# Kernel tuning notes

Measured on AMD Instinct MI355X. Metric: run time of the kernel, lower is better.

Reference implementation:

```python
import jax, jax.numpy as jnp
import numpy as np
import math

HIDDEN = 2048
NUM_HEADS = 16
HEAD_DIM = HIDDEN // NUM_HEADS  # 128
B, T = 2, 2048
MAX_POS = 4096
ROPE_BASE = 10000.0


def _rope_cache(dim, max_pos, base):
    inv_freq = 1.0 / (base ** (jnp.arange(0, dim, 2, dtype=jnp.float32) / dim))
    t = jnp.arange(max_pos, dtype=jnp.float32)
    freqs = jnp.einsum('i,j->ij', t, inv_freq)        # [max_pos, dim/2]
    emb = jnp.concatenate([freqs, freqs], axis=-1)     # [max_pos, dim]
    return jnp.cos(emb), jnp.sin(emb)


def setup_inputs() -> dict:
    key = jax.random.key(0)
    ks = jax.random.split(key, 5)
    hidden_states = jax.random.normal(ks[0], (B, T, HIDDEN), dtype=jnp.float32)
    # additive causal mask, large negative (not -inf) for numerical safety
    causal = jnp.triu(jnp.full((T, T), -1e9, dtype=jnp.float32), k=1)
    attention_mask = causal[None, None, :, :]          # [1,1,T,T]
    position_ids = jnp.arange(T, dtype=jnp.int64)
    s = 1.0 / math.sqrt(HIDDEN)
    Wq = jax.random.normal(ks[1], (HIDDEN, HIDDEN), dtype=jnp.float32) * s
    Wk = jax.random.normal(ks[2], (HIDDEN, HIDDEN), dtype=jnp.float32) * s
    Wv = jax.random.normal(ks[3], (HIDDEN, HIDDEN), dtype=jnp.float32) * s
    Wo = jax.random.normal(ks[4], (HIDDEN, HIDDEN), dtype=jnp.float32) * s
    cos_cached, sin_cached = _rope_cache(HEAD_DIM, MAX_POS, ROPE_BASE)
    return {
        'hidden_states': hidden_states,
        'attention_mask': attention_mask,
        'position_ids': position_ids,
        'Wq': Wq, 'Wk': Wk, 'Wv': Wv, 'Wo': Wo,
        'cos_cached': cos_cached, 'sin_cached': sin_cached,
    }


def _apply_rope(x, cos, sin):
    # x: [B, T, nh, hd]; cos/sin: [T, 1, hd] (broadcast over heads)
    x1 = x[..., 0::2]
    x2 = x[..., 1::2]
    x_rot = jnp.stack([-x2, x1], axis=-1).reshape(x.shape)  # interleaved rotate
    return x * cos + x_rot * sin


def reference(hidden_states, attention_mask, position_ids, Wq, Wk, Wv, Wo,
              cos_cached, sin_cached):
    Bs, Ts, H = hidden_states.shape
    nh, hd = NUM_HEADS, HEAD_DIM
    q = (hidden_states @ Wq.T).reshape(Bs, Ts, nh, hd)
    k = (hidden_states @ Wk.T).reshape(Bs, Ts, nh, hd)
    v = (hidden_states @ Wv.T).reshape(Bs, Ts, nh, hd)
    cos = cos_cached[position_ids][:, None, :]  # [T,1,hd]
    sin = sin_cached[position_ids][:, None, :]
    q = _apply_rope(q, cos, sin)
    k = _apply_rope(k, cos, sin)
    # [B, nh, T, hd]
    q = q.transpose(0, 2, 1, 3)
    k = k.transpose(0, 2, 1, 3)
    v = v.transpose(0, 2, 1, 3)
    scores = jnp.einsum('bhqd,bhkd->bhqk', q, k) / math.sqrt(hd)
    scores = scores + attention_mask
    attn = jax.nn.softmax(scores, axis=-1)
    out = jnp.einsum('bhqk,bhkd->bhqd', attn, v)
    out = out.transpose(0, 2, 1, 3).reshape(Bs, Ts, H)
    return out @ Wo.T
```

## Files before the change

### kernel.cpp

```cpp
#include <hip/hip_runtime.h>
#include <cstdint>


typedef __bf16 v8bf __attribute__((ext_vector_type(8)));
typedef float  v4f  __attribute__((ext_vector_type(4)));
typedef float  f32x16 __attribute__((ext_vector_type(16)));

__device__ __forceinline__ uint16_t f2bf(float f) {
  union { float f; uint32_t u; } v; v.f = f;
  uint32_t u = v.u;
  return (uint16_t)((u + 0x7FFFu + ((u >> 16) & 1u)) >> 16);
}

__device__ __forceinline__ uint32_t cvtpk(float lo, float hi) {
  uint32_t w;
  asm("v_cvt_pk_bf16_f32 %0, %1, %2" : "=v"(w) : "v"(lo), "v"(hi));
  return w;
}

__device__ __forceinline__ void gload16(const void* g, void* l) {
  __builtin_amdgcn_global_load_lds(
      (const __attribute__((address_space(1))) void*)g,
      (__attribute__((address_space(3))) void*)l, 16, 0, 0);
}

__global__ void cvt_all_kernel(const float* __restrict__ s0, uint16_t* d0,
                               const float* __restrict__ s1, uint16_t* d1,
                               const float* __restrict__ s2, uint16_t* d2,
                               const float* __restrict__ s3, uint16_t* d3,
                               const float* __restrict__ s4, uint16_t* d4) {
  const float* src; uint16_t* dst; int n4;
  switch (blockIdx.y) {
    case 0: src = s0; dst = d0; n4 = 2097152; break;
    case 1: src = s1; dst = d1; n4 = 1048576; break;
    case 2: src = s2; dst = d2; n4 = 1048576; break;
    case 3: src = s3; dst = d3; n4 = 1048576; break;
    default: src = s4; dst = d4; n4 = 1048576; break;
  }
  int i = blockIdx.x * blockDim.x + threadIdx.x;
  int stride = gridDim.x * blockDim.x;
  for (; i < n4; i += stride) {
    float4 v = reinterpret_cast<const float4*>(src)[i];
    ushort4 o;
    o.x = f2bf(v.x); o.y = f2bf(v.y); o.z = f2bf(v.z); o.w = f2bf(v.w);
    reinterpret_cast<ushort4*>(dst)[i] = o;
  }
}

__device__ __forceinline__ void gemm128_mainloop(
    const uint16_t* __restrict__ A, const uint16_t* __restrict__ Bt,
    int m0, int n0, uint16_t* As, uint16_t* Bs, v4f acc[4][4]) {
  const int tid  = threadIdx.x;
  const int lane = tid & 63;
  const int w    = tid >> 6;
  const int wr   = w >> 1, wc = w & 1;
  const int lrow = lane & 15;
  const int lhi  = lane >> 4;

  auto stage = [&](int buf, int k0) {
    uint16_t* Ad = As + buf * 8192;
    uint16_t* Bd = Bs + buf * 8192;
#pragma unroll
    for (int i = 0; i < 4; ++i) {
      int c = i * 256 + tid;
      int row = c >> 3, seg = c & 7;
      int sseg = seg ^ (row & 7);
      gload16(A + (size_t)(m0 + row) * 2048 + k0 + sseg * 8, Ad + c * 8);
    }
#pragma unroll
    for (int i = 0; i < 4; ++i) {
      int c = i * 256 + tid;
      int row = c >> 3, seg = c & 7;
      int sseg = seg ^ (row & 7);
      gload16(Bt + (size_t)(n0 + row) * 2048 + k0 + sseg * 8, Bd + c * 8);
    }
  };

  stage(0, 0);
  for (int t = 0; t < 32; ++t) {
    __syncthreads();
    if (t + 1 < 32) stage((t + 1) & 1, (t + 1) * 64);
    const uint16_t* Ac = As + (t & 1) * 8192;
    const uint16_t* Bc = Bs + (t & 1) * 8192;
#pragma unroll
    for (int ks = 0; ks < 2; ++ks) {
      v8bf af[4], bfv[4];
#pragma unroll
      for (int mf = 0; mf < 4; ++mf) {
        const int ar = wr * 64 + mf * 16 + lrow;
        const int seg = (ks * 4 + lhi) ^ (ar & 7);
        af[mf] = *reinterpret_cast<const v8bf*>(Ac + ar * 64 + seg * 8);
      }
#pragma unroll
      for (int nf = 0; nf < 4; ++nf) {
        const int br = wc * 64 + nf * 16 + lrow;
        const int seg = (ks * 4 + lhi) ^ (br & 7);
        bfv[nf] = *reinterpret_cast<const v8bf*>(Bc + br * 64 + seg * 8);
      }
#pragma unroll
      for (int mf = 0; mf < 4; ++mf)
#pragma unroll
        for (int nf = 0; nf < 4; ++nf)
          acc[mf][nf] = __builtin_amdgcn_mfma_f32_16x16x32_bf16(
              af[mf], bfv[nf], acc[mf][nf], 0, 0, 0);
    }
  }
}

__global__ __launch_bounds__(256, 2) void qkv_gemm_kernel(
    const uint16_t* __restrict__ Xbf,
    const uint16_t* __restrict__ Wqb, const uint16_t* __restrict__ Wkb,
    const uint16_t* __restrict__ Wvb,
    const float* __restrict__ cosc, const float* __restrict__ sinc,
    uint16_t* __restrict__ Qh, uint16_t* __restrict__ Kh,
    uint16_t* __restrict__ Vt) {
  __shared__ uint16_t As[2 * 128 * 64];
  __shared__ uint16_t Bs[2 * 128 * 64];
  const int id  = (blockIdx.z * 32 + blockIdx.y) * 16 + blockIdx.x;
  const int swz = (id & 7) * 192 + (id >> 3);
  const int which = swz >> 9;
  const int m0 = ((swz >> 4) & 31) * 128, n0 = (swz & 15) * 128;
  const uint16_t* Wb = (which == 0) ? Wqb : (which == 1) ? Wkb : Wvb;

  v4f acc[4][4];
#pragma unroll
  for (int i = 0; i < 4; ++i)
#pragma unroll
    for (int j = 0; j < 4; ++j) acc[i][j] = (v4f)0.0f;

  gemm128_mainloop(Xbf, Wb, m0, n0, As, Bs, acc);

  const int lane = threadIdx.x & 63;
  const int w = threadIdx.x >> 6, wr = w >> 1, wc = w & 1;
  const int lrow = lane & 15, lhi = lane >> 4;
  const int b = m0 >> 11;

  if (which < 2) {
    uint16_t* dst = (which == 0) ? Qh : Kh;
#pragma unroll
    for (int mf = 0; mf < 4; ++mf) {
#pragma unroll
      for (int nf = 0; nf < 4; ++nf) {
        const int n = n0 + wc * 64 + nf * 16 + lrow;
        const int head = n >> 7, d = n & 127;
#pragma unroll
        for (int r = 0; r < 4; ++r) {
          const int m = m0 + wr * 64 + mf * 16 + lhi * 4 + r;
          const int t = m & 2047;
          float v = acc[mf][nf][r];
          float p = __shfl_xor(v, 1);
          float rot = (n & 1) ? p : -p;
          float cf = cosc[t * 128 + d], sf = sinc[t * 128 + d];
          dst[((size_t)(b * 16 + head) * 2048 + t) * 128 + d] =
              f2bf(v * cf + rot * sf);
        }
      }
    }
  } else {
#pragma unroll
    for (int mf = 0; mf < 4; ++mf) {
#pragma unroll
      for (int nf = 0; nf < 4; ++nf) {
        const int n = n0 + wc * 64 + nf * 16 + lrow;
        const int head = n >> 7, d = n & 127;
        const int m = m0 + wr * 64 + mf * 16 + lhi * 4;
        const int t = m & 2047;
        ushort4 o;
        o.x = f2bf(acc[mf][nf][0]); o.y = f2bf(acc[mf][nf][1]);
        o.z = f2bf(acc[mf][nf][2]); o.w = f2bf(acc[mf][nf][3]);
        *reinterpret_cast<ushort4*>(
            &Vt[((size_t)(b * 16 + head) * 128 + d) * 2048 + t]) = o;
      }
    }
  }
}

__global__ __launch_bounds__(256, 2) void attn_kernel(
    const uint16_t* __restrict__ Qh, const uint16_t* __restrict__ Kh,
    const uint16_t* __restrict__ Vt, uint16_t* __restrict__ Ob) {
  __shared__ uint16_t Ks[2 * 64 * 128];
  __shared__ uint16_t Vs[2 * 128 * 64];

  const int id = blockIdx.x;
  const int qt = (id < 256) ? (15 - (id >> 5)) : ((id - 256) >> 5);
  const int bh = id & 31;
  const int tid = threadIdx.x, lane = tid & 63, w = tid >> 6;
  const int l31 = lane & 31, hi = lane >> 5;
  const size_t base = (size_t)bh * 2048 * 128;
  const int q0 = qt * 128 + w * 32;
  const int qr = q0 + l31;

  v8bf qf[8];
#pragma unroll
  for (int ks = 0; ks < 8; ++ks)
    qf[ks] = *reinterpret_cast<const v8bf*>(
        Qh + base + (size_t)qr * 128 + ks * 16 + hi * 8);

  f32x16 acc[4];
#pragma unroll
  for (int d = 0; d < 4; ++d) acc[d] = (f32x16)0.0f;
  float m = -1e30f, l = 0.0f;

  auto stage = [&](int buf, int kt) {
    uint16_t* Kd = Ks + buf * 8192;
    uint16_t* Vd = Vs + buf * 8192;
#pragma unroll
    for (int i = 0; i < 4; ++i) {
      int c = i * 256 + tid;
      int row = c >> 4, seg = c & 15;
      int sseg = seg ^ (row & 7);
      gload16(Kh + base + (size_t)(kt * 64 + row) * 128 + sseg * 8,
              Kd + c * 8);
    }
#pragma unroll
    for (int i = 0; i < 4; ++i) {
      int c = i * 256 + tid;
      int row = c >> 3, seg = c & 7;
      int sseg = seg ^ (row & 7);
      gload16(Vt + base + (size_t)row * 2048 + kt * 64 + sseg * 8,
              Vd + c * 8);
    }
  };

  const float sc = 0.08838834764831845f;
  const int nkt = 2 * (qt + 1);
  stage(0, 0);
  for (int kt = 0; kt < nkt; ++kt) {
    const int cur = kt & 1;
    __syncthreads();
    if (kt + 1 < nkt) stage(cur ^ 1, kt + 1);
    const uint16_t* Kc = Ks + cur * 8192;
    const uint16_t* Vc = Vs + cur * 8192;

    if (kt * 64 <= q0 + 31) {
      f32x16 s[2];
      s[0] = (f32x16)0.0f; s[1] = (f32x16)0.0f;
#pragma unroll
      for (int kb = 0; kb < 2; ++kb) {
        const int row = kb * 32 + l31;
        const int swz = row & 7;
#pragma unroll
        for (int ks = 0; ks < 8; ++ks) {
          const int seg = (ks * 2 + hi) ^ swz;
          v8bf kf = *reinterpret_cast<const v8bf*>(Kc + row * 128 + seg * 8);
          s[kb] = __builtin_amdgcn_mfma_f32_32x32x16_bf16(kf, qf[ks], s[kb],
                                                          0, 0, 0);
        }
      }
      if (kt * 64 + 63 > q0) {
#pragma unroll
        for (int kb = 0; kb < 2; ++kb)
#pragma unroll
          for (int q = 0; q < 4; ++q)
#pragma unroll
            for (int r = 0; r < 4; ++r) {
              const int kc = kt * 64 + kb * 32 + q * 8 + hi * 4 + r;
              float v = s[kb][q * 4 + r] * sc;
              s[kb][q * 4 + r] = (kc > qr) ? -1e30f : v;
            }
      } else {
#pragma unroll
        for (int kb = 0; kb < 2; ++kb)
#pragma unroll
          for (int g = 0; g < 16; ++g) s[kb][g] *= sc;
      }
      float t8[8];
#pragma unroll
      for (int g = 0; g < 8; ++g)
        t8[g] = fmaxf(fmaxf(s[0][g], s[0][g + 8]),
                      fmaxf(s[1][g], s[1][g + 8]));
      float mx = fmaxf(fmaxf(fmaxf(t8[0], t8[1]), fmaxf(t8[2], t8[3])),
                       fmaxf(fmaxf(t8[4], t8[5]), fmaxf(t8[6], t8[7])));
      mx = fmaxf(mx, __shfl_xor(mx, 32));
      if (!__all(mx - m <= 8.0f)) {
        const float mnew = fmaxf(m, mx);
        const float so = __expf(m - mnew);
        m = mnew;
        l *= so;
#pragma unroll
        for (int d = 0; d < 4; ++d)
#pragma unroll
          for (int g = 0; g < 16; ++g) acc[d][g] *= so;
      }
      float rs = 0.0f;
#pragma unroll
      for (int kb = 0; kb < 2; ++kb)
#pragma unroll
        for (int g = 0; g < 16; ++g) {
          const float pv = __expf(s[kb][g] - m);
          s[kb][g] = pv;
          rs += pv;
        }
      rs += __shfl_xor(rs, 32);
      l += rs;
      union BW { uint32_t w[4]; v8bf v; };
      BW pb[4];
#pragma unroll
      for (int kb = 0; kb < 2; ++kb)
#pragma unroll
        for (int sl = 0; sl < 2; ++sl) {
          uint32_t a0 = cvtpk(s[kb][8 * sl + 0], s[kb][8 * sl + 1]);
          uint32_t a1 = cvtpk(s[kb][8 * sl + 2], s[kb][8 * sl + 3]);
          uint32_t b0 = cvtpk(s[kb][8 * sl + 4], s[kb][8 * sl + 5]);
          uint32_t b1 = cvtpk(s[kb][8 * sl + 6], s[kb][8 * sl + 7]);
          asm("v_permlane32_swap_b32 %0, %1" : "+v"(a0), "+v"(b0));
          asm("v_permlane32_swap_b32 %0, %1" : "+v"(a1), "+v"(b1));
          BW& f = pb[kb * 2 + sl];
          f.w[0] = a0; f.w[1] = a1; f.w[2] = b0; f.w[3] = b1;
        }
#pragma unroll
      for (int d = 0; d < 4; ++d) {
        const int row = d * 32 + l31;
        const int swz = row & 7;
#pragma unroll
        for (int sl4 = 0; sl4 < 4; ++sl4) {
          const int seg = (sl4 * 2 + hi) ^ swz;
          v8bf va = *reinterpret_cast<const v8bf*>(Vc + row * 64 + seg * 8);
          acc[d] = __builtin_amdgcn_mfma_f32_32x32x16_bf16(va, pb[sl4].v,
                                                           acc[d], 0, 0, 0);
        }
      }
    }
  }

  const int b = bh >> 4, head = bh & 15;
  const float inv = 1.0f / l;
#pragma unroll
  for (int d = 0; d < 4; ++d)
#pragma unroll
    for (int q = 0; q < 4; ++q)
#pragma unroll
      for (int rp = 0; rp < 2; ++rp) {
        const int dd = d * 32 + q * 8 + hi * 4 + rp * 2;
        const uint32_t lo16 = f2bf(acc[d][q * 4 + rp * 2] * inv);
        const uint32_t hi16 = f2bf(acc[d][q * 4 + rp * 2 + 1] * inv);
        *reinterpret_cast<uint32_t*>(
            &Ob[((size_t)(b * 2048 + qr)) * 2048 + head * 128 + dd]) =
            lo16 | (hi16 << 16);
      }
}

__global__ __launch_bounds__(256, 2) void out_gemm_kernel(
    const uint16_t* __restrict__ Abf, const uint16_t* __restrict__ Wob,
    float* __restrict__ out) {
  __shared__ uint16_t As[2 * 128 * 64];
  __shared__ uint16_t Bs[2 * 128 * 64];
  const int id  = blockIdx.y * 16 + blockIdx.x;
  const int swz = (id & 7) * 64 + (id >> 3);
  const int m0 = (swz >> 4) * 128, n0 = (swz & 15) * 128;
  v4f acc[4][4];
#pragma unroll
  for (int i = 0; i < 4; ++i)
#pragma unroll
    for (int j = 0; j < 4; ++j) acc[i][j] = (v4f)0.0f;

  gemm128_mainloop(Abf, Wob, m0, n0, As, Bs, acc);

  const int lane = threadIdx.x & 63;
  const int w = threadIdx.x >> 6, wr = w >> 1, wc = w & 1;
  const int lrow = lane & 15, lhi = lane >> 4;
#pragma unroll
  for (int mf = 0; mf < 4; ++mf)
#pragma unroll
    for (int nf = 0; nf < 4; ++nf) {
      const int n = n0 + wc * 64 + nf * 16 + lrow;
#pragma unroll
      for (int r = 0; r < 4; ++r) {
        const int m = m0 + wr * 64 + mf * 16 + lhi * 4 + r;
        out[(size_t)m * 2048 + n] = acc[mf][nf][r];
      }
    }
}

extern "C" void kernel_launch(void* const* d_in, const int* in_sizes, int n_in,
                              void* d_out, int out_size, void* d_ws,
                              size_t ws_size, hipStream_t stream) {
  const float* hidden = (const float*)d_in[0];
  const float* Wq = (const float*)d_in[3];
  const float* Wk = (const float*)d_in[4];
  const float* Wv = (const float*)d_in[5];
  const float* Wo = (const float*)d_in[6];
  const float* cosc = (const float*)d_in[7];
  const float* sinc = (const float*)d_in[8];
  float* out = (float*)d_out;

  uint16_t* Wqb = (uint16_t*)d_ws;
  uint16_t* Wkb = Wqb + 4194304;
  uint16_t* Wvb = Wkb + 4194304;
  uint16_t* Wob = Wvb + 4194304;
  uint16_t* Xbf = Wob + 4194304;
  uint16_t* Qh  = Xbf + 8388608;
  uint16_t* Kh  = Qh + 8388608;
  uint16_t* Vt  = Kh + 8388608;
  uint16_t* Ob  = Xbf;

  cvt_all_kernel<<<dim3(512, 5), 256, 0, stream>>>(
      hidden, Xbf, Wq, Wqb, Wk, Wkb, Wv, Wvb, Wo, Wob);

  qkv_gemm_kernel<<<dim3(16, 32, 3), 256, 0, stream>>>(
      Xbf, Wqb, Wkb, Wvb, cosc, sinc, Qh, Kh, Vt);

  attn_kernel<<<dim3(512), 256, 0, stream>>>(Qh, Kh, Vt, Ob);

  out_gemm_kernel<<<dim3(16, 32), 256, 0, stream>>>(Ob, Wob, out);
}
```

Before: 408.9 us.

## Enlarge GEMM tiles with triple-buffered pipeline; shrink attention KV tiles and stage output via LDS

The GEMMs switch to 256x128 tiles with 512 threads and a three-stage LDS ring. Loads are split across the two k-substeps with explicit vmcnt waits, barriers and setprio around the MFMA block, to overlap global loads with compute and raise reuse. Attention moves to 32-key tiles with a three-buffer ring and explicit waitcnt. Its output goes through a swizzled LDS transpose so each row is written to global memory in coalesced form. The risks are higher LDS use limiting occupancy (the GEMMs need 144KB of LDS at 2 blocks per CU), and more barrier overhead per attention tile.

New measurement: 381.2 us. 1.07x faster.

```diff
diff --git a/kernel.cpp b/kernel.cpp
--- a/kernel.cpp
+++ b/kernel.cpp
@@ -47,79 +47,104 @@
   }
 }
 
-__device__ __forceinline__ void gemm128_mainloop(
+__device__ __forceinline__ void gemm256_mainloop(
     const uint16_t* __restrict__ A, const uint16_t* __restrict__ Bt,
     int m0, int n0, uint16_t* As, uint16_t* Bs, v4f acc[4][4]) {
   const int tid  = threadIdx.x;
-  const int lane = tid & 63;
-  const int w    = tid >> 6;
-  const int wr   = w >> 1, wc = w & 1;
-  const int lrow = lane & 15;
-  const int lhi  = lane >> 4;
-
-  auto stage = [&](int buf, int k0) {
-    uint16_t* Ad = As + buf * 8192;
-    uint16_t* Bd = Bs + buf * 8192;
-#pragma unroll
-    for (int i = 0; i < 4; ++i) {
-      int c = i * 256 + tid;
-      int row = c >> 3, seg = c & 7;
-      int sseg = seg ^ (row & 7);
-      gload16(A + (size_t)(m0 + row) * 2048 + k0 + sseg * 8, Ad + c * 8);
-    }
-#pragma unroll
-    for (int i = 0; i < 4; ++i) {
-      int c = i * 256 + tid;
-      int row = c >> 3, seg = c & 7;
-      int sseg = seg ^ (row & 7);
-      gload16(Bt + (size_t)(n0 + row) * 2048 + k0 + sseg * 8, Bd + c * 8);
-    }
+  const int lane = tid & 63, w = tid >> 6;
+  const int wm = w >> 1, wn = w & 1;
+  const int lrow = lane & 15, lhi = lane >> 4;
+
+  auto stageA = [&](int buf, int k0, int i) {
+    int c = i * 512 + tid;
+    int row = c >> 3, seg = c & 7;
+    int sseg = seg ^ (row & 7);
+    gload16(A + (size_t)(m0 + row) * 2048 + k0 + sseg * 8,
+            As + buf * 16384 + c * 8);
   };
-
-  stage(0, 0);
+  auto stageB = [&](int buf, int k0, int i) {
+    int c = i * 512 + tid;
+    int row = c >> 3, seg = c & 7;
+    int sseg = seg ^ (row & 7);
+    gload16(Bt + (size_t)(n0 + row) * 2048 + k0 + sseg * 8,
+            Bs + buf * 8192 + c * 8);
+  };
+
+#pragma unroll
+  for (int i = 0; i < 4; ++i) stageA(0, 0, i);
+#pragma unroll
+  for (int i = 0; i < 2; ++i) stageB(0, 0, i);
+#pragma unroll
+  for (int i = 0; i < 4; ++i) stageA(1, 64, i);
+#pragma unroll
+  for (int i = 0; i < 2; ++i) stageB(1, 64, i);
+  asm volatile("s_waitcnt vmcnt(6)" ::: "memory");
+  __builtin_amdgcn_s_barrier();
+  __builtin_amdgcn_sched_barrier(0);
+
   for (int t = 0; t < 32; ++t) {
-    __syncthreads();
-    if (t + 1 < 32) stage((t + 1) & 1, (t + 1) * 64);
-    const uint16_t* Ac = As + (t & 1) * 8192;
-    const uint16_t* Bc = Bs + (t & 1) * 8192;
+    const int cb = t % 3;
+    const int sb = (t + 2) % 3;
+    const int sk = (t + 2) * 64;
+    const uint16_t* Ac = As + cb * 16384;
+    const uint16_t* Bc = Bs + cb * 8192;
+    const bool do_stage = (t + 2) < 32;
 #pragma unroll
     for (int ks = 0; ks < 2; ++ks) {
       v8bf af[4], bfv[4];
 #pragma unroll
       for (int mf = 0; mf < 4; ++mf) {
-        const int ar = wr * 64 + mf * 16 + lrow;
+        const int ar = wm * 64 + mf * 16 + lrow;
         const int seg = (ks * 4 + lhi) ^ (ar & 7);
         af[mf] = *reinterpret_cast<const v8bf*>(Ac + ar * 64 + seg * 8);
       }
 #pragma unroll
       for (int nf = 0; nf < 4; ++nf) {
-        const int br = wc * 64 + nf * 16 + lrow;
+        const int br = wn * 64 + nf * 16 + lrow;
         const int seg = (ks * 4 + lhi) ^ (br & 7);
         bfv[nf] = *reinterpret_cast<const v8bf*>(Bc + br * 64 + seg * 8);
       }
+      if (do_stage) {
+        if (ks == 0) { stageA(sb, sk, 0); stageA(sb, sk, 1); stageB(sb, sk, 0); }
+        else         { stageA(sb, sk, 2); stageA(sb, sk, 3); stageB(sb, sk, 1); }
+      }
+      if (ks == 1) {
+        if (t < 30) asm volatile("s_waitcnt vmcnt(6)" ::: "memory");
+        else        asm volatile("s_waitcnt vmcnt(0)" ::: "memory");
+      } else {
+        asm volatile("" ::: "memory");
+      }
+      __builtin_amdgcn_s_barrier();
+      __builtin_amdgcn_sched_barrier(0);
+      __builtin_amdgcn_s_setprio(1);
 #pragma unroll
       for (int mf = 0; mf < 4; ++mf)
 #pragma unroll
         for (int nf = 0; nf < 4; ++nf)
           acc[mf][nf] = __builtin_amdgcn_mfma_f32_16x16x32_bf16(
               af[mf], bfv[nf], acc[mf][nf], 0, 0, 0);
-    }
-  }
-}
-
-__global__ __launch_bounds__(256, 2) void qkv_gemm_kernel(
+      __builtin_amdgcn_s_setprio(0);
+      asm volatile("" ::: "memory");
+      __builtin_amdgcn_s_barrier();
+      __builtin_amdgcn_sched_barrier(0);
+    }
+  }
+}
+
+__global__ __launch_bounds__(512, 2) void qkv_gemm_kernel(
     const uint16_t* __restrict__ Xbf,
     const uint16_t* __restrict__ Wqb, const uint16_t* __restrict__ Wkb,
     const uint16_t* __restrict__ Wvb,
     const float* __restrict__ cosc, const float* __restrict__ sinc,
     uint16_t* __restrict__ Qh, uint16_t* __restrict__ Kh,
     uint16_t* __restrict__ Vt) {
-  __shared__ uint16_t As[2 * 128 * 64];
-  __shared__ uint16_t Bs[2 * 128 * 64];
-  const int id  = (blockIdx.z * 32 + blockIdx.y) * 16 + blockIdx.x;
-  const int swz = (id & 7) * 192 + (id >> 3);
-  const int which = swz >> 9;
-  const int m0 = ((swz >> 4) & 31) * 128, n0 = (swz & 15) * 128;
+  __shared__ uint16_t As[3 * 256 * 64];
+  __shared__ uint16_t Bs[3 * 128 * 64];
+  const int id  = blockIdx.x;
+  const int swz = (id & 7) * 96 + (id >> 3);
+  const int which = swz >> 8;
+  const int rem = swz & 255;
+  const int m0 = (rem >> 4) * 256, n0 = (rem & 15) * 128;
   const uint16_t* Wb = (which == 0) ? Wqb : (which == 1) ? Wkb : Wvb;
 
   v4f acc[4][4];
@@ -128,10 +153,10 @@
 #pragma unroll
     for (int j = 0; j < 4; ++j) acc[i][j] = (v4f)0.0f;
 
-  gemm128_mainloop(Xbf, Wb, m0, n0, As, Bs, acc);
+  gemm256_mainloop(Xbf, Wb, m0, n0, As, Bs, acc);
 
   const int lane = threadIdx.x & 63;
-  const int w = threadIdx.x >> 6, wr = w >> 1, wc = w & 1;
+  const int w = threadIdx.x >> 6, wm = w >> 1, wn = w & 1;
   const int lrow = lane & 15, lhi = lane >> 4;
   const int b = m0 >> 11;
 
@@ -141,11 +166,11 @@
     for (int mf = 0; mf < 4; ++mf) {
 #pragma unroll
       for (int nf = 0; nf < 4; ++nf) {
-        const int n = n0 + wc * 64 + nf * 16 + lrow;
+        const int n = n0 + wn * 64 + nf * 16 + lrow;
         const int head = n >> 7, d = n & 127;
 #pragma unroll
         for (int r = 0; r < 4; ++r) {
-          const int m = m0 + wr * 64 + mf * 16 + lhi * 4 + r;
+          const int m = m0 + wm * 64 + mf * 16 + lhi * 4 + r;
           const int t = m & 2047;
           float v = acc[mf][nf][r];
           float p = __shfl_xor(v, 1);
@@ -161,9 +186,9 @@
     for (int mf = 0; mf < 4; ++mf) {
 #pragma unroll
       for (int nf = 0; nf < 4; ++nf) {
-        const int n = n0 + wc * 64 + nf * 16 + lrow;
+        const int n = n0 + wn * 64 + nf * 16 + lrow;
         const int head = n >> 7, d = n & 127;
-        const int m = m0 + wr * 64 + mf * 16 + lhi * 4;
+        const int m = m0 + wm * 64 + mf * 16 + lhi * 4;
         const int t = m & 2047;
         ushort4 o;
         o.x = f2bf(acc[mf][nf][0]); o.y = f2bf(acc[mf][nf][1]);
@@ -178,8 +203,7 @@
 __global__ __launch_bounds__(256, 2) void attn_kernel(
     const uint16_t* __restrict__ Qh, const uint16_t* __restrict__ Kh,
     const uint16_t* __restrict__ Vt, uint16_t* __restrict__ Ob) {
-  __shared__ uint16_t Ks[2 * 64 * 128];
-  __shared__ uint16_t Vs[2 * 128 * 64];
+  __shared__ uint16_t KV[3][8192];
 
   const int id = blockIdx.x;
   const int qt = (id < 256) ? (15 - (id >> 5)) : ((id - 256) >> 5);
@@ -202,73 +226,67 @@
   float m = -1e30f, l = 0.0f;
 
   auto stage = [&](int buf, int kt) {
-    uint16_t* Kd = Ks + buf * 8192;
-    uint16_t* Vd = Vs + buf * 8192;
-#pragma unroll
-    for (int i = 0; i < 4; ++i) {
+    uint16_t* Kd = KV[buf];
+    uint16_t* Vd = KV[buf] + 4096;
+#pragma unroll
+    for (int i = 0; i < 2; ++i) {
       int c = i * 256 + tid;
       int row = c >> 4, seg = c & 15;
       int sseg = seg ^ (row & 7);
-      gload16(Kh + base + (size_t)(kt * 64 + row) * 128 + sseg * 8,
+      gload16(Kh + base + (size_t)(kt * 32 + row) * 128 + sseg * 8,
               Kd + c * 8);
     }
 #pragma unroll
-    for (int i = 0; i < 4; ++i) {
+    for (int i = 0; i < 2; ++i) {
       int c = i * 256 + tid;
-      int row = c >> 3, seg = c & 7;
-      int sseg = seg ^ (row & 7);
-      gload16(Vt + base + (size_t)row * 2048 + kt * 64 + sseg * 8,
+      int row = c >> 2, seg = c & 3;
+      int sseg = seg ^ (row & 3);
+      gload16(Vt + base + (size_t)row * 2048 + kt * 32 + sseg * 8,
               Vd + c * 8);
     }
   };
 
   const float sc = 0.08838834764831845f;
-  const int nkt = 2 * (qt + 1);
+  const int nkt = 4 * (qt + 1);
   stage(0, 0);
+  stage(1, 1);
   for (int kt = 0; kt < nkt; ++kt) {
-    const int cur = kt & 1;
-    __syncthreads();
-    if (kt + 1 < nkt) stage(cur ^ 1, kt + 1);
-    const uint16_t* Kc = Ks + cur * 8192;
-    const uint16_t* Vc = Vs + cur * 8192;
-
-    if (kt * 64 <= q0 + 31) {
-      f32x16 s[2];
-      s[0] = (f32x16)0.0f; s[1] = (f32x16)0.0f;
-#pragma unroll
-      for (int kb = 0; kb < 2; ++kb) {
-        const int row = kb * 32 + l31;
-        const int swz = row & 7;
+    const int cb = kt % 3;
+    if (kt + 1 < nkt) asm volatile("s_waitcnt vmcnt(4)" ::: "memory");
+    else              asm volatile("s_waitcnt vmcnt(0)" ::: "memory");
+    __builtin_amdgcn_s_barrier();
+    __builtin_amdgcn_sched_barrier(0);
+    if (kt + 2 < nkt) stage((kt + 2) % 3, kt + 2);
+
+    if (kt * 32 <= q0 + 31) {
+      const uint16_t* Kc = KV[cb];
+      const uint16_t* Vc = KV[cb] + 4096;
+      f32x16 s = (f32x16)0.0f;
+      {
+        const int swzk = l31 & 7;
 #pragma unroll
         for (int ks = 0; ks < 8; ++ks) {
-          const int seg = (ks * 2 + hi) ^ swz;
-          v8bf kf = *reinterpret_cast<const v8bf*>(Kc + row * 128 + seg * 8);
-          s[kb] = __builtin_amdgcn_mfma_f32_32x32x16_bf16(kf, qf[ks], s[kb],
-                                                          0, 0, 0);
+          const int seg = (ks * 2 + hi) ^ swzk;
+          v8bf kf = *reinterpret_cast<const v8bf*>(Kc + l31 * 128 + seg * 8);
+          s = __builtin_amdgcn_mfma_f32_32x32x16_bf16(kf, qf[ks], s, 0, 0, 0);
         }
       }
-      if (kt * 64 + 63 > q0) {
-#pragma unroll
-        for (int kb = 0; kb < 2; ++kb)
-#pragma unroll
-          for (int q = 0; q < 4; ++q)
-#pragma unroll
-            for (int r = 0; r < 4; ++r) {
-              const int kc = kt * 64 + kb * 32 + q * 8 + hi * 4 + r;
-              float v = s[kb][q * 4 + r] * sc;
-              s[kb][q * 4 + r] = (kc > qr) ? -1e30f : v;
-            }
+      if (kt * 32 + 31 > q0) {
+#pragma unroll
+        for (int q = 0; q < 4; ++q)
+#pragma unroll
+          for (int r = 0; r < 4; ++r) {
+            const int kc = kt * 32 + q * 8 + hi * 4 + r;
+            float v = s[q * 4 + r] * sc;
+            s[q * 4 + r] = (kc > qr) ? -1e30f : v;
+          }
       } else {
 #pragma unroll
-        for (int kb = 0; kb < 2; ++kb)
-#pragma unroll
-          for (int g = 0; g < 16; ++g) s[kb][g] *= sc;
+        for (int g = 0; g < 16; ++g) s[g] *= sc;
       }
       float t8[8];
 #pragma unroll
-      for (int g = 0; g < 8; ++g)
-        t8[g] = fmaxf(fmaxf(s[0][g], s[0][g + 8]),
-                      fmaxf(s[1][g], s[1][g + 8]));
+      for (int g = 0; g < 8; ++g) t8[g] = fmaxf(s[g], s[g + 8]);
       float mx = fmaxf(fmaxf(fmaxf(t8[0], t8[1]), fmaxf(t8[2], t8[3])),
                        fmaxf(fmaxf(t8[4], t8[5]), fmaxf(t8[6], t8[7])));
       mx = fmaxf(mx, __shfl_xor(mx, 32));
@@ -284,46 +302,44 @@
       }
       float rs = 0.0f;
 #pragma unroll
-      for (int kb = 0; kb < 2; ++kb)
-#pragma unroll
-        for (int g = 0; g < 16; ++g) {
-          const float pv = __expf(s[kb][g] - m);
-          s[kb][g] = pv;
-          rs += pv;
-        }
+      for (int g = 0; g < 16; ++g) {
+        const float pv = __expf(s[g] - m);
+        s[g] = pv;
+        rs += pv;
+      }
       rs += __shfl_xor(rs, 32);
       l += rs;
       union BW { uint32_t w[4]; v8bf v; };
-      BW pb[4];
-#pragma unroll
-      for (int kb = 0; kb < 2; ++kb)
-#pragma unroll
-        for (int sl = 0; sl < 2; ++sl) {
-          uint32_t a0 = cvtpk(s[kb][8 * sl + 0], s[kb][8 * sl + 1]);
-          uint32_t a1 = cvtpk(s[kb][8 * sl + 2], s[kb][8 * sl + 3]);
-          uint32_t b0 = cvtpk(s[kb][8 * sl + 4], s[kb][8 * sl + 5]);
-          uint32_t b1 = cvtpk(s[kb][8 * sl + 6], s[kb][8 * sl + 7]);
-          asm("v_permlane32_swap_b32 %0, %1" : "+v"(a0), "+v"(b0));
-          asm("v_permlane32_swap_b32 %0, %1" : "+v"(a1), "+v"(b1));
-          BW& f = pb[kb * 2 + sl];
-          f.w[0] = a0; f.w[1] = a1; f.w[2] = b0; f.w[3] = b1;
-        }
+      BW pb[2];
+#pragma unroll
+      for (int sl = 0; sl < 2; ++sl) {
+        uint32_t a0 = cvtpk(s[8 * sl + 0], s[8 * sl + 1]);
+        uint32_t a1 = cvtpk(s[8 * sl + 2], s[8 * sl + 3]);
+        uint32_t b0 = cvtpk(s[8 * sl + 4], s[8 * sl + 5]);
+        uint32_t b1 = cvtpk(s[8 * sl + 6], s[8 * sl + 7]);
+        asm("v_permlane32_swap_b32 %0, %1" : "+v"(a0), "+v"(b0));
+        asm("v_permlane32_swap_b32 %0, %1" : "+v"(a1), "+v"(b1));
+        pb[sl].w[0] = a0; pb[sl].w[1] = a1; pb[sl].w[2] = b0; pb[sl].w[3] = b1;
+      }
+      const int swzv = l31 & 3;
 #pragma unroll
       for (int d = 0; d < 4; ++d) {
         const int row = d * 32 + l31;
-        const int swz = row & 7;
-#pragma unroll
-        for (int sl4 = 0; sl4 < 4; ++sl4) {
-          const int seg = (sl4 * 2 + hi) ^ swz;
-          v8bf va = *reinterpret_cast<const v8bf*>(Vc + row * 64 + seg * 8);
-          acc[d] = __builtin_amdgcn_mfma_f32_32x32x16_bf16(va, pb[sl4].v,
+#pragma unroll
+        for (int sl = 0; sl < 2; ++sl) {
+          const int seg = (sl * 2 + hi) ^ swzv;
+          v8bf va = *reinterpret_cast<const v8bf*>(Vc + row * 32 + seg * 8);
+          acc[d] = __builtin_amdgcn_mfma_f32_32x32x16_bf16(va, pb[sl].v,
                                                            acc[d], 0, 0, 0);
         }
       }
     }
   }
 
-  const int b = bh >> 4, head = bh & 15;
+  asm volatile("s_waitcnt vmcnt(0) lgkmcnt(0)" ::: "memory");
+  __builtin_amdgcn_s_barrier();
+  __builtin_amdgcn_sched_barrier(0);
+  uint32_t* L32 = reinterpret_cast<uint32_t*>(&KV[0][0]);
   const float inv = 1.0f / l;
 #pragma unroll
   for (int d = 0; d < 4; ++d)
@@ -331,42 +347,52 @@
     for (int q = 0; q < 4; ++q)
 #pragma unroll
       for (int rp = 0; rp < 2; ++rp) {
-        const int dd = d * 32 + q * 8 + hi * 4 + rp * 2;
+        const int dd1 = d * 16 + q * 4 + hi * 2 + rp;
         const uint32_t lo16 = f2bf(acc[d][q * 4 + rp * 2] * inv);
         const uint32_t hi16 = f2bf(acc[d][q * 4 + rp * 2 + 1] * inv);
-        *reinterpret_cast<uint32_t*>(
-            &Ob[((size_t)(b * 2048 + qr)) * 2048 + head * 128 + dd]) =
+        L32[(w * 32 + l31) * 64 + (dd1 ^ ((l31 & 7) << 3))] =
             lo16 | (hi16 << 16);
       }
-}
-
-__global__ __launch_bounds__(256, 2) void out_gemm_kernel(
+  asm volatile("" ::: "memory");
+  __builtin_amdgcn_s_barrier();
+  __builtin_amdgcn_sched_barrier(0);
+  const int b = bh >> 4, head = bh & 15;
+  uint32_t* Og = reinterpret_cast<uint32_t*>(Ob);
+#pragma unroll
+  for (int j = 0; j < 32; ++j) {
+    const int qrow = qt * 128 + w * 32 + j;
+    const uint32_t v = L32[(w * 32 + j) * 64 + (lane ^ ((j & 7) << 3))];
+    Og[((size_t)(b * 2048 + qrow) * 2048 + head * 128) / 2 + lane] = v;
+  }
+}
+
+__global__ __launch_bounds__(512, 2) void out_gemm_kernel(
     const uint16_t* __restrict__ Abf, const uint16_t* __restrict__ Wob,
     float* __restrict__ out) {
-  __shared__ uint16_t As[2 * 128 * 64];
-  __shared__ uint16_t Bs[2 * 128 * 64];
-  const int id  = blockIdx.y * 16 + blockIdx.x;
-  const int swz = (id & 7) * 64 + (id >> 3);
-  const int m0 = (swz >> 4) * 128, n0 = (swz & 15) * 128;
+  __shared__ uint16_t As[3 * 256 * 64];
+  __shared__ uint16_t Bs[3 * 128 * 64];
+  const int id  = blockIdx.x;
+  const int swz = (id & 7) * 32 + (id >> 3);
+  const int m0 = (swz >> 4) * 256, n0 = (swz & 15) * 128;
   v4f acc[4][4];
 #pragma unroll
   for (int i = 0; i < 4; ++i)
 #pragma unroll
     for (int j = 0; j < 4; ++j) acc[i][j] = (v4f)0.0f;
 
-  gemm128_mainloop(Abf, Wob, m0, n0, As, Bs, acc);
+  gemm256_mainloop(Abf, Wob, m0, n0, As, Bs, acc);
 
   const int lane = threadIdx.x & 63;
-  const int w = threadIdx.x >> 6, wr = w >> 1, wc = w & 1;
+  const int w = threadIdx.x >> 6, wm = w >> 1, wn = w & 1;
   const int lrow = lane & 15, lhi = lane >> 4;
 #pragma unroll
   for (int mf = 0; mf < 4; ++mf)
 #pragma unroll
     for (int nf = 0; nf < 4; ++nf) {
-      const int n = n0 + wc * 64 + nf * 16 + lrow;
+      const int n = n0 + wn * 64 + nf * 16 + lrow;
 #pragma unroll
       for (int r = 0; r < 4; ++r) {
-        const int m = m0 + wr * 64 + mf * 16 + lhi * 4 + r;
+        const int m = m0 + wm * 64 + mf * 16 + lhi * 4 + r;
         out[(size_t)m * 2048 + n] = acc[mf][nf][r];
       }
     }
@@ -397,10 +423,10 @@
   cvt_all_kernel<<<dim3(512, 5), 256, 0, stream>>>(
       hidden, Xbf, Wq, Wqb, Wk, Wkb, Wv, Wvb, Wo, Wob);
 
-  qkv_gemm_kernel<<<dim3(16, 32, 3), 256, 0, stream>>>(
+  qkv_gemm_kernel<<<dim3(768), 512, 0, stream>>>(
       Xbf, Wqb, Wkb, Wvb, cosc, sinc, Qh, Kh, Vt);
 
   attn_kernel<<<dim3(512), 256, 0, stream>>>(Qh, Kh, Vt, Ob);
 
-  out_gemm_kernel<<<dim3(16, 32), 256, 0, stream>>>(Ob, Wob, out);
-}
+  out_gemm_kernel<<<dim3(256), 512, 0, stream>>>(Ob, Wob, out);
+}
```
